# Performance work log

Hardware: AMD Instinct MI355X
Metric: run time of the kernel (lower is better)

The kernel has to match this reference:

```python
import jax, jax.numpy as jnp
import numpy as np

B, H = 32, 1024  # seq_len == hidden_size (required by the original code's shapes)
S = H

def setup_inputs() -> dict:
    key = jax.random.key(0)
    k1, k2, k3, k4, k5 = jax.random.split(key, 5)
    hidden = jax.random.normal(k1, (B, H), dtype=jnp.float32)
    encoder_outputs = jax.random.normal(k2, (B, S, H), dtype=jnp.float32)
    # nn.Linear(2H -> H): weight [H, 2H], bias [H]
    lim = 1.0 / np.sqrt(2 * H)
    W = jax.random.uniform(k3, (H, 2 * H), dtype=jnp.float32, minval=-lim, maxval=lim)
    b = jax.random.uniform(k4, (H,), dtype=jnp.float32, minval=-lim, maxval=lim)
    # v ~ Normal(0, 1/H)
    v = jax.random.normal(k5, (H,), dtype=jnp.float32) * (1.0 / H)
    return {"hidden": hidden, "encoder_outputs": encoder_outputs, "W": W, "b": b, "v": v}

def reference(hidden, encoder_outputs, W, b, v):
    # hidden: [B, H]; encoder_outputs: [B, S, H] with S == H
    S_len = encoder_outputs.shape[1]
    h_rep = jnp.broadcast_to(hidden[:, None, :], (hidden.shape[0], S_len, hidden.shape[1]))
    enc_t = jnp.swapaxes(encoder_outputs, 1, 2)  # [B, H, S] == [B, S, H] (square)
    x = jnp.concatenate([h_rep, enc_t], axis=2)  # [B, S, 2H]
    energy = jnp.tanh(jnp.einsum('bsk,hk->bsh', x, W) + b)  # [B, S, H]
    # scores[b,s] = sum_h v[h] * energy[b,s,h], softmax over s
    scores = jax.nn.softmax(jnp.einsum('h,bsh->bs', v, energy), axis=1)  # [B, S]
    # bmm(scores[B,1,S], enc_t.transpose(1,2)=encoder_outputs[B,S,H]) -> [B, H]
    context = jnp.einsum('bs,bsh->bh', scores, encoder_outputs)
    return context, scores[:, None, :]
```

## Files before the change

### kernel.cpp

```cpp
#include <hip/hip_runtime.h>
#include <hip/hip_bf16.h>
#include <math.h>

#define B_ 32
#define H_ 1024
#define S_ 1024

typedef float  f32x4_t  __attribute__((ext_vector_type(4)));
typedef float  f32x16_t __attribute__((ext_vector_type(16)));
typedef long long i64;
typedef i64 i64x2 __attribute__((ext_vector_type(2)));
typedef unsigned char u8;

__device__ __forceinline__ void gl_lds16(const void* g, void* l) {
    __builtin_amdgcn_global_load_lds(
        (const __attribute__((address_space(1))) unsigned int*)g,
        (__attribute__((address_space(3))) unsigned int*)l, 16, 0, 0);
}

__device__ __forceinline__ float tanh_fast(float x) {
    float e = __builtin_amdgcn_exp2f(x * 2.885390081777927f);
    return 1.f - 2.f * __builtin_amdgcn_rcpf(e + 1.f);
}

__device__ __forceinline__ int kperm(int k) {
    return (k & ~24) | ((k & 8) << 1) | ((k & 16) >> 1);
}

__global__ __launch_bounds__(256) void prep_kernel(
    const float* __restrict__ enc, const float* __restrict__ W,
    const float* __restrict__ hidden, const float* __restrict__ bias,
    u8* __restrict__ encF8, u8* __restrict__ W2f8,
    float* __restrict__ t1, float* __restrict__ logits,
    float* __restrict__ ctx)
{
    const int idx = blockIdx.x;
    const int tid = threadIdx.x;
    if (idx < 4096) {
        const int b  = idx >> 7;
        const int r  = idx & 127;
        const int kt = r >> 2;
        const int sb = (r & 3) * 256;
        const int s4 = tid >> 2;
        const int g  = (tid >> 1) & 1;
        const int c  = tid & 1;
        const int s  = sb + s4 * 4;
        const int row0 = kt * 32 + g * 16 + c * 8;
        const float* ebase = enc + ((size_t)b * S_ + row0) * H_ + s;
        f32x4_t L0 = *reinterpret_cast<const f32x4_t*>(ebase);
        f32x4_t L1 = *reinterpret_cast<const f32x4_t*>(ebase + H_);
        f32x4_t L2 = *reinterpret_cast<const f32x4_t*>(ebase + 2 * H_);
        f32x4_t L3 = *reinterpret_cast<const f32x4_t*>(ebase + 3 * H_);
        f32x4_t L4 = *reinterpret_cast<const f32x4_t*>(ebase + 4 * H_);
        f32x4_t L5 = *reinterpret_cast<const f32x4_t*>(ebase + 5 * H_);
        f32x4_t L6 = *reinterpret_cast<const f32x4_t*>(ebase + 6 * H_);
        f32x4_t L7 = *reinterpret_cast<const f32x4_t*>(ebase + 7 * H_);
        u8* obase = encF8 + (size_t)b * 1048576 + (size_t)kt * 32768
                  + (size_t)s * 32 + c * 16 + g * 8;
        #pragma unroll
        for (int jj = 0; jj < 4; ++jj) {
            int w0 = __builtin_amdgcn_cvt_pk_fp8_f32(L0[jj], L1[jj], 0, false);
            w0     = __builtin_amdgcn_cvt_pk_fp8_f32(L2[jj], L3[jj], w0, true);
            int w1 = __builtin_amdgcn_cvt_pk_fp8_f32(L4[jj], L5[jj], 0, false);
            w1     = __builtin_amdgcn_cvt_pk_fp8_f32(L6[jj], L7[jj], w1, true);
            int2 payload = { w0, w1 };
            *reinterpret_cast<int2*>(obase + jj * 32) = payload;
        }
    } else if (idx < 5120) {
        int h = idx - 4096;
        if (tid < 64) {
            int z = h * 64 + tid;
            if (z < B_ * S_) logits[z] = 0.f;
            else             ctx[z - B_ * S_] = 0.f;
        }
        int kt = tid >> 3;
        int q  = tid & 7;
        int src = kperm(q * 4);
        float4 wv = *reinterpret_cast<const float4*>(
            W + (size_t)h * (2 * H_) + H_ + kt * 32 + src);
        int pw = __builtin_amdgcn_cvt_pk_fp8_f32(wv.x * 64.f, wv.y * 64.f, 0, false);
        pw     = __builtin_amdgcn_cvt_pk_fp8_f32(wv.z * 64.f, wv.w * 64.f, pw, true);
        *reinterpret_cast<int*>(W2f8 + (size_t)kt * 32768 + (size_t)h * 32 + q * 4) = pw;
    } else {
        int h    = (idx - 5120) * 4 + (tid >> 6);
        int lane = tid & 63;
        const float4* wp = reinterpret_cast<const float4*>(W + (size_t)h * (2 * H_));
        float4 w0 = wp[lane], w1 = wp[lane + 64], w2 = wp[lane + 128], w3 = wp[lane + 192];
        float bh = bias[h];
        for (int b = 0; b < B_; ++b) {
            const float4* hp = reinterpret_cast<const float4*>(hidden + b * H_);
            float4 h0 = hp[lane], h1 = hp[lane + 64], h2 = hp[lane + 128], h3 = hp[lane + 192];
            float a = w0.x*h0.x + w0.y*h0.y + w0.z*h0.z + w0.w*h0.w
                    + w1.x*h1.x + w1.y*h1.y + w1.z*h1.z + w1.w*h1.w
                    + w2.x*h2.x + w2.y*h2.y + w2.z*h2.z + w2.w*h2.w
                    + w3.x*h3.x + w3.y*h3.y + w3.z*h3.z + w3.w*h3.w;
            #pragma unroll
            for (int off = 1; off < 64; off <<= 1) a += __shfl_xor(a, off);
            if (lane == 0) t1[b * H_ + h] = a + bh;
        }
    }
}

__global__ __launch_bounds__(256) void energy_kernel(
    const u8* __restrict__ W2f8, const u8* __restrict__ encF8,
    const float* __restrict__ t1, const float* __restrict__ v,
    float* __restrict__ logits)
{
    __shared__ __align__(16) u8 As[2][2][4096];
    __shared__ __align__(16) u8 Bs[2][2][4096];

    const int id = blockIdx.x;
    const int q  = id >> 3, r = id & 7;
    const int ht = q & 7;
    const int g  = r + ((q >> 3) << 3);
    const int b  = g >> 3;
    const int h0 = ht * 128;
    const int s0 = (g & 7) * 128;

    const int tid   = threadIdx.x;
    const int lane  = tid & 63;
    const int wid   = tid >> 6;
    const int wm    = (wid & 1) * 64;
    const int wn    = (wid >> 1) * 64;
    const int l32   = lane & 31;
    const int khalf = lane >> 5;

    const int rowl = ((lane & 3) << 3) | ((lane >> 2) & 7);
    const int row  = (wid << 5) | rowl;
    const int cch  = lane >> 5;
    const size_t gofsA = (size_t)(h0 + row) * 32 + cch * 16;
    const size_t gofsB = (size_t)b * 1048576 + (size_t)(s0 + row) * 32 + cch * 16;

    gl_lds16(W2f8 + gofsA,          &As[0][0][tid * 16]);
    gl_lds16(W2f8 + gofsA + 32768,  &As[0][1][tid * 16]);
    gl_lds16(encF8 + gofsB,         &Bs[0][0][tid * 16]);
    gl_lds16(encF8 + gofsB + 32768, &Bs[0][1][tid * 16]);
    __syncthreads();

    f32x16_t acc[2][2] = {};
    const int sl  = ((((l32 & 7) << 2) | (l32 >> 3)) | (khalf << 5)) * 16;
    const int wAo = (wm >> 5) * 1024;
    const int wBo = (wn >> 5) * 1024;

    for (int seg = 0; seg < 16; ++seg) {
        const int cur = seg & 1, nxt = cur ^ 1;
        if (seg < 15) {
            const size_t o = (size_t)(2 * seg + 2) * 32768;
            gl_lds16(W2f8 + gofsA + o,          &As[nxt][0][tid * 16]);
            gl_lds16(W2f8 + gofsA + o + 32768,  &As[nxt][1][tid * 16]);
            gl_lds16(encF8 + gofsB + o,         &Bs[nxt][0][tid * 16]);
            gl_lds16(encF8 + gofsB + o + 32768, &Bs[nxt][1][tid * 16]);
        }
        #pragma unroll
        for (int t = 0; t < 2; ++t) {
            i64x2 a0 = *reinterpret_cast<const i64x2*>(&As[cur][t][wAo + sl]);
            i64x2 a1 = *reinterpret_cast<const i64x2*>(&As[cur][t][wAo + 1024 + sl]);
            i64x2 b0 = *reinterpret_cast<const i64x2*>(&Bs[cur][t][wBo + sl]);
            i64x2 b1 = *reinterpret_cast<const i64x2*>(&Bs[cur][t][wBo + 1024 + sl]);
            acc[0][0] = __builtin_amdgcn_mfma_f32_32x32x16_fp8_fp8(a0.x, b0.x, acc[0][0], 0, 0, 0);
            acc[0][1] = __builtin_amdgcn_mfma_f32_32x32x16_fp8_fp8(a0.x, b1.x, acc[0][1], 0, 0, 0);
            acc[1][0] = __builtin_amdgcn_mfma_f32_32x32x16_fp8_fp8(a1.x, b0.x, acc[1][0], 0, 0, 0);
            acc[1][1] = __builtin_amdgcn_mfma_f32_32x32x16_fp8_fp8(a1.x, b1.x, acc[1][1], 0, 0, 0);
            acc[0][0] = __builtin_amdgcn_mfma_f32_32x32x16_fp8_fp8(a0.y, b0.y, acc[0][0], 0, 0, 0);
            acc[0][1] = __builtin_amdgcn_mfma_f32_32x32x16_fp8_fp8(a0.y, b1.y, acc[0][1], 0, 0, 0);
            acc[1][0] = __builtin_amdgcn_mfma_f32_32x32x16_fp8_fp8(a1.y, b0.y, acc[1][0], 0, 0, 0);
            acc[1][1] = __builtin_amdgcn_mfma_f32_32x32x16_fp8_fp8(a1.y, b1.y, acc[1][1], 0, 0, 0);
        }
        __syncthreads();
    }

    float pn0 = 0.f, pn1 = 0.f;
    #pragma unroll
    for (int mt = 0; mt < 2; ++mt)
        #pragma unroll
        for (int rr = 0; rr < 16; ++rr) {
            int rowm = wm + mt * 32 + (rr & 3) + 8 * (rr >> 2) + 4 * khalf;
            int h = h0 + rowm;
            float tv = t1[b * H_ + h];
            float vv = v[h];
            pn0 += vv * tanh_fast(acc[mt][0][rr] * 0.015625f + tv);
            pn1 += vv * tanh_fast(acc[mt][1][rr] * 0.015625f + tv);
        }
    pn0 += __shfl_xor(pn0, 32);
    pn1 += __shfl_xor(pn1, 32);
    if (lane < 32) {
        atomicAdd(&logits[(size_t)b * S_ + s0 + wn + l32], pn0);
        atomicAdd(&logits[(size_t)b * S_ + s0 + wn + 32 + l32], pn1);
    }
}

__global__ __launch_bounds__(256) void ctx_kernel(
    const float* __restrict__ enc, const float* __restrict__ logits,
    float* __restrict__ scores, float* __restrict__ ctx)
{
    __shared__ float sc[1024];
    __shared__ float red[8];
    const int b    = blockIdx.y;
    const int s0   = blockIdx.x * 64;
    const int tid  = threadIdx.x;
    const int lane = tid & 63;
    const int w    = tid >> 6;

    float4 lg = *reinterpret_cast<const float4*>(logits + (size_t)b * S_ + tid * 4);
    float mx = fmaxf(fmaxf(lg.x, lg.y), fmaxf(lg.z, lg.w));
    #pragma unroll
    for (int off = 1; off < 64; off <<= 1) mx = fmaxf(mx, __shfl_xor(mx, off));
    if (lane == 0) red[w] = mx;
    __syncthreads();
    mx = fmaxf(fmaxf(red[0], red[1]), fmaxf(red[2], red[3]));
    const float L2E = 1.44269504088896f;
    float e0 = __builtin_amdgcn_exp2f((lg.x - mx) * L2E);
    float e1 = __builtin_amdgcn_exp2f((lg.y - mx) * L2E);
    float e2 = __builtin_amdgcn_exp2f((lg.z - mx) * L2E);
    float e3 = __builtin_amdgcn_exp2f((lg.w - mx) * L2E);
    float s = e0 + e1 + e2 + e3;
    #pragma unroll
    for (int off = 1; off < 64; off <<= 1) s += __shfl_xor(s, off);
    if (lane == 0) red[4 + w] = s;
    __syncthreads();
    float inv = 1.f / (red[4] + red[5] + red[6] + red[7]);
    float4 sv = { e0 * inv, e1 * inv, e2 * inv, e3 * inv };
    *reinterpret_cast<float4*>(&sc[tid * 4]) = sv;
    if (blockIdx.x == 0)
        *reinterpret_cast<float4*>(scores + (size_t)b * S_ + tid * 4) = sv;
    __syncthreads();

    f32x4_t accv = {0.f, 0.f, 0.f, 0.f};
    const float* ebase = enc + ((size_t)b * S_ + s0) * H_ + tid * 4;
    #pragma unroll 4
    for (int si = 0; si < 64; ++si) {
        float wgt = sc[s0 + si];
        float4 ev = *reinterpret_cast<const float4*>(ebase + (size_t)si * H_);
        accv[0] += wgt * ev.x;
        accv[1] += wgt * ev.y;
        accv[2] += wgt * ev.z;
        accv[3] += wgt * ev.w;
    }
    float* cp = ctx + (size_t)b * H_ + tid * 4;
    atomicAdd(cp + 0, accv[0]);
    atomicAdd(cp + 1, accv[1]);
    atomicAdd(cp + 2, accv[2]);
    atomicAdd(cp + 3, accv[3]);
}

extern "C" void kernel_launch(void* const* d_in, const int* in_sizes, int n_in,
                              void* d_out, int out_size, void* d_ws, size_t ws_size,
                              hipStream_t stream)
{
    (void)in_sizes; (void)n_in; (void)out_size; (void)ws_size;
    const float* hidden = (const float*)d_in[0];
    const float* enc    = (const float*)d_in[1];
    const float* W      = (const float*)d_in[2];
    const float* bias   = (const float*)d_in[3];
    const float* v      = (const float*)d_in[4];

    float* out    = (float*)d_out;
    float* ctx    = out;
    float* scores = out + B_ * H_;

    float* logits = (float*)d_ws;
    float* t1     = logits + B_ * S_;
    u8*    W2f8   = (u8*)(t1 + B_ * H_);
    u8*    encF8  = W2f8 + (size_t)H_ * H_;

    prep_kernel<<<dim3(4096 + 1024 + 256), 256, 0, stream>>>(
        enc, W, hidden, bias, encF8, W2f8, t1, logits, ctx);
    energy_kernel<<<dim3(2048), 256, 0, stream>>>(W2f8, encF8, t1, v, logits);
    ctx_kernel<<<dim3(S_ / 64, B_), 256, 0, stream>>>(enc, logits, scores, ctx);
}
```

Measured before the change: 315.2 us.

## Load MFMA operands directly from global into registers, dropping LDS staging

The energy GEMM no longer stages W2 and encoder fp8 tiles through double-buffered shared memory with global_load_lds and block barriers. Each lane now loads its MFMA operand fragments straight from global memory into registers, prefetching the next K-slice one step ahead. This removes the LDS round trip and the per-segment __syncthreads. In exchange each A/B fragment is fetched separately by the two waves that share it, which relies on L1/L2 to absorb the duplicate reads, and latency hiding is only one iteration deep.

```diff
diff --git a/kernel.cpp b/kernel.cpp
--- a/kernel.cpp
+++ b/kernel.cpp
@@ -11,12 +11,6 @@
 typedef long long i64;
 typedef i64 i64x2 __attribute__((ext_vector_type(2)));
 typedef unsigned char u8;
-
-__device__ __forceinline__ void gl_lds16(const void* g, void* l) {
-    __builtin_amdgcn_global_load_lds(
-        (const __attribute__((address_space(1))) unsigned int*)g,
-        (__attribute__((address_space(3))) unsigned int*)l, 16, 0, 0);
-}
 
 __device__ __forceinline__ float tanh_fast(float x) {
     float e = __builtin_amdgcn_exp2f(x * 2.885390081777927f);
@@ -106,9 +100,6 @@
     const float* __restrict__ t1, const float* __restrict__ v,
     float* __restrict__ logits)
 {
-    __shared__ __align__(16) u8 As[2][2][4096];
-    __shared__ __align__(16) u8 Bs[2][2][4096];
-
     const int id = blockIdx.x;
     const int q  = id >> 3, r = id & 7;
     const int ht = q & 7;
@@ -125,49 +116,45 @@
     const int l32   = lane & 31;
     const int khalf = lane >> 5;
 
-    const int rowl = ((lane & 3) << 3) | ((lane >> 2) & 7);
-    const int row  = (wid << 5) | rowl;
-    const int cch  = lane >> 5;
-    const size_t gofsA = (size_t)(h0 + row) * 32 + cch * 16;
-    const size_t gofsB = (size_t)b * 1048576 + (size_t)(s0 + row) * 32 + cch * 16;
-
-    gl_lds16(W2f8 + gofsA,          &As[0][0][tid * 16]);
-    gl_lds16(W2f8 + gofsA + 32768,  &As[0][1][tid * 16]);
-    gl_lds16(encF8 + gofsB,         &Bs[0][0][tid * 16]);
-    gl_lds16(encF8 + gofsB + 32768, &Bs[0][1][tid * 16]);
-    __syncthreads();
+    const u8* aP = W2f8 + (size_t)(h0 + wm + l32) * 32 + khalf * 16;
+    const u8* bP = encF8 + (size_t)b * 1048576
+                 + (size_t)(s0 + wn + l32) * 32 + khalf * 16;
 
     f32x16_t acc[2][2] = {};
-    const int sl  = ((((l32 & 7) << 2) | (l32 >> 3)) | (khalf << 5)) * 16;
-    const int wAo = (wm >> 5) * 1024;
-    const int wBo = (wn >> 5) * 1024;
-
-    for (int seg = 0; seg < 16; ++seg) {
-        const int cur = seg & 1, nxt = cur ^ 1;
-        if (seg < 15) {
-            const size_t o = (size_t)(2 * seg + 2) * 32768;
-            gl_lds16(W2f8 + gofsA + o,          &As[nxt][0][tid * 16]);
-            gl_lds16(W2f8 + gofsA + o + 32768,  &As[nxt][1][tid * 16]);
-            gl_lds16(encF8 + gofsB + o,         &Bs[nxt][0][tid * 16]);
-            gl_lds16(encF8 + gofsB + o + 32768, &Bs[nxt][1][tid * 16]);
-        }
-        #pragma unroll
-        for (int t = 0; t < 2; ++t) {
-            i64x2 a0 = *reinterpret_cast<const i64x2*>(&As[cur][t][wAo + sl]);
-            i64x2 a1 = *reinterpret_cast<const i64x2*>(&As[cur][t][wAo + 1024 + sl]);
-            i64x2 b0 = *reinterpret_cast<const i64x2*>(&Bs[cur][t][wBo + sl]);
-            i64x2 b1 = *reinterpret_cast<const i64x2*>(&Bs[cur][t][wBo + 1024 + sl]);
-            acc[0][0] = __builtin_amdgcn_mfma_f32_32x32x16_fp8_fp8(a0.x, b0.x, acc[0][0], 0, 0, 0);
-            acc[0][1] = __builtin_amdgcn_mfma_f32_32x32x16_fp8_fp8(a0.x, b1.x, acc[0][1], 0, 0, 0);
-            acc[1][0] = __builtin_amdgcn_mfma_f32_32x32x16_fp8_fp8(a1.x, b0.x, acc[1][0], 0, 0, 0);
-            acc[1][1] = __builtin_amdgcn_mfma_f32_32x32x16_fp8_fp8(a1.x, b1.x, acc[1][1], 0, 0, 0);
-            acc[0][0] = __builtin_amdgcn_mfma_f32_32x32x16_fp8_fp8(a0.y, b0.y, acc[0][0], 0, 0, 0);
-            acc[0][1] = __builtin_amdgcn_mfma_f32_32x32x16_fp8_fp8(a0.y, b1.y, acc[0][1], 0, 0, 0);
-            acc[1][0] = __builtin_amdgcn_mfma_f32_32x32x16_fp8_fp8(a1.y, b0.y, acc[1][0], 0, 0, 0);
-            acc[1][1] = __builtin_amdgcn_mfma_f32_32x32x16_fp8_fp8(a1.y, b1.y, acc[1][1], 0, 0, 0);
-        }
-        __syncthreads();
-    }
+
+    i64x2 ca0 = *reinterpret_cast<const i64x2*>(aP);
+    i64x2 ca1 = *reinterpret_cast<const i64x2*>(aP + 1024);
+    i64x2 cb0 = *reinterpret_cast<const i64x2*>(bP);
+    i64x2 cb1 = *reinterpret_cast<const i64x2*>(bP + 1024);
+    const u8* aN = aP + 32768;
+    const u8* bN = bP + 32768;
+
+    for (int kt = 0; kt < 31; ++kt) {
+        i64x2 na0 = *reinterpret_cast<const i64x2*>(aN);
+        i64x2 na1 = *reinterpret_cast<const i64x2*>(aN + 1024);
+        i64x2 nb0 = *reinterpret_cast<const i64x2*>(bN);
+        i64x2 nb1 = *reinterpret_cast<const i64x2*>(bN + 1024);
+        aN += 32768; bN += 32768;
+
+        acc[0][0] = __builtin_amdgcn_mfma_f32_32x32x16_fp8_fp8(ca0.x, cb0.x, acc[0][0], 0, 0, 0);
+        acc[0][1] = __builtin_amdgcn_mfma_f32_32x32x16_fp8_fp8(ca0.x, cb1.x, acc[0][1], 0, 0, 0);
+        acc[1][0] = __builtin_amdgcn_mfma_f32_32x32x16_fp8_fp8(ca1.x, cb0.x, acc[1][0], 0, 0, 0);
+        acc[1][1] = __builtin_amdgcn_mfma_f32_32x32x16_fp8_fp8(ca1.x, cb1.x, acc[1][1], 0, 0, 0);
+        acc[0][0] = __builtin_amdgcn_mfma_f32_32x32x16_fp8_fp8(ca0.y, cb0.y, acc[0][0], 0, 0, 0);
+        acc[0][1] = __builtin_amdgcn_mfma_f32_32x32x16_fp8_fp8(ca0.y, cb1.y, acc[0][1], 0, 0, 0);
+        acc[1][0] = __builtin_amdgcn_mfma_f32_32x32x16_fp8_fp8(ca1.y, cb0.y, acc[1][0], 0, 0, 0);
+        acc[1][1] = __builtin_amdgcn_mfma_f32_32x32x16_fp8_fp8(ca1.y, cb1.y, acc[1][1], 0, 0, 0);
+
+        ca0 = na0; ca1 = na1; cb0 = nb0; cb1 = nb1;
+    }
+    acc[0][0] = __builtin_amdgcn_mfma_f32_32x32x16_fp8_fp8(ca0.x, cb0.x, acc[0][0], 0, 0, 0);
+    acc[0][1] = __builtin_amdgcn_mfma_f32_32x32x16_fp8_fp8(ca0.x, cb1.x, acc[0][1], 0, 0, 0);
+    acc[1][0] = __builtin_amdgcn_mfma_f32_32x32x16_fp8_fp8(ca1.x, cb0.x, acc[1][0], 0, 0, 0);
+    acc[1][1] = __builtin_amdgcn_mfma_f32_32x32x16_fp8_fp8(ca1.x, cb1.x, acc[1][1], 0, 0, 0);
+    acc[0][0] = __builtin_amdgcn_mfma_f32_32x32x16_fp8_fp8(ca0.y, cb0.y, acc[0][0], 0, 0, 0);
+    acc[0][1] = __builtin_amdgcn_mfma_f32_32x32x16_fp8_fp8(ca0.y, cb1.y, acc[0][1], 0, 0, 0);
+    acc[1][0] = __builtin_amdgcn_mfma_f32_32x32x16_fp8_fp8(ca1.y, cb0.y, acc[1][0], 0, 0, 0);
+    acc[1][1] = __builtin_amdgcn_mfma_f32_32x32x16_fp8_fp8(ca1.y, cb1.y, acc[1][1], 0, 0, 0);
 
     float pn0 = 0.f, pn1 = 0.f;
     #pragma unroll
```

Result: faster. 297.3 us (-5.7%).
